# Performance work log

Hardware: AMD Instinct MI355X
Metric: run time of the kernel (lower is better)

The kernel has to match this reference:

```python
import jax, jax.numpy as jnp
import numpy as np

N_NODES = 100000
N_EDGES = 1600000
D_IN = 128
D_HID = 128
D_OUT = 128
N_GRAPHS = 64


def setup_inputs() -> dict:
    key = jax.random.key(0)
    ks = jax.random.split(key, 10)
    x = jax.random.normal(ks[0], (N_NODES, D_IN), dtype=jnp.float32)
    edge_index = jax.random.randint(ks[1], (2, N_EDGES), 0, N_NODES, dtype=jnp.int64)
    graph_id = jnp.sort(jax.random.randint(ks[2], (N_NODES,), 0, N_GRAPHS, dtype=jnp.int64))
    s1 = 1.0 / np.sqrt(D_IN)
    s2 = 1.0 / np.sqrt(D_HID)
    s3 = 1.0 / np.sqrt(D_OUT)
    W1 = jax.random.normal(ks[3], (D_IN, D_HID), dtype=jnp.float32) * s1
    b1 = jnp.zeros((D_HID,), dtype=jnp.float32)
    W2 = jax.random.normal(ks[4], (D_HID, D_OUT), dtype=jnp.float32) * s2
    b2 = jnp.zeros((D_OUT,), dtype=jnp.float32)
    Wr1 = jax.random.normal(ks[5], (D_OUT, D_OUT), dtype=jnp.float32) * s3
    br1 = jnp.zeros((D_OUT,), dtype=jnp.float32)
    Wr2 = jax.random.normal(ks[6], (D_OUT, D_OUT), dtype=jnp.float32) * s3
    br2 = jnp.zeros((D_OUT,), dtype=jnp.float32)
    return {"x": x, "edge_index": edge_index, "graph_id": graph_id,
            "num_graphs": N_GRAPHS, "W1": W1, "b1": b1, "W2": W2, "b2": b2,
            "Wr1": Wr1, "br1": br1, "Wr2": Wr2, "br2": br2}


def _graph_conv(h, W, b, src, dst, norm_src, norm_dst, n_nodes):
    # DGL GraphConv, norm='both': out = D_dst^{-1/2} A (D_src^{-1/2} h) W + b
    h = h * norm_src[:, None]
    h = h @ W  # project first (cheap, keeps SpMM on the smaller/equal dim)
    agg = jax.ops.segment_sum(h[src], dst, num_segments=n_nodes)
    return agg * norm_dst[:, None] + b


def reference(x, edge_index, graph_id, num_graphs, W1, b1, W2, b2, Wr1, br1, Wr2, br2):
    src, dst = edge_index[0], edge_index[1]
    n_nodes = x.shape[0]
    ones = jnp.ones((src.shape[0],), dtype=x.dtype)
    deg_out = jax.ops.segment_sum(ones, src, num_segments=n_nodes)
    deg_in = jax.ops.segment_sum(ones, dst, num_segments=n_nodes)
    norm_src = jnp.clip(deg_out, 1.0) ** -0.5
    norm_dst = jnp.clip(deg_in, 1.0) ** -0.5

    # layer 1 + relu (dropout is identity in eval mode)
    h = _graph_conv(x, W1, b1, src, dst, norm_src, norm_dst, n_nodes)
    h = jax.nn.relu(h)
    # layer 2 + relu
    h = _graph_conv(h, W2, b2, src, dst, norm_src, norm_dst, n_nodes)
    h = jax.nn.relu(h)

    # per-graph mean pooling (dgl.mean_nodes)
    sums = jax.ops.segment_sum(h, graph_id, num_segments=num_graphs)
    counts = jax.ops.segment_sum(jnp.ones((n_nodes,), dtype=h.dtype), graph_id,
                                 num_segments=num_graphs)
    hg = sums / jnp.clip(counts, 1.0)[:, None]

    # readout MLP: Linear -> ReLU -> Linear
    out = jax.nn.relu(hg @ Wr1 + br1) @ Wr2 + br2
    return (out, h)
```

## Files before the change

### kernel.cpp

```cpp
#include <hip/hip_runtime.h>
#include <math.h>


#define D 128
#define BSH 8
#define BKT 256
#define CAP 4608
#define SCHUNK 3200

typedef _Float16 half8 __attribute__((ext_vector_type(8)));
typedef _Float16 half4v __attribute__((ext_vector_type(4)));
typedef _Float16 half2v __attribute__((ext_vector_type(2)));
typedef float f32x4 __attribute__((ext_vector_type(4)));

union H8 { half8 v; half2v h[4]; };

__global__ __launch_bounds__(512) void k_build(const int* __restrict__ src,
                                               const int* __restrict__ dst,
                                               int* __restrict__ cnt_d,
                                               int* __restrict__ cnt_s,
                                               int* __restrict__ packed_d,
                                               unsigned char* __restrict__ packed_s8,
                                               const float* __restrict__ W1,
                                               const float* __restrict__ W2,
                                               _Float16* __restrict__ Wt1,
                                               _Float16* __restrict__ Wt2,
                                               const int* __restrict__ gid,
                                               int* __restrict__ gptr,
                                               int N, int E, int nbkt) {
  __shared__ int hd[512], hs[512], exd[512], exs[512], based[512], bases[512];
  __shared__ int sd[SCHUNK];
  __shared__ unsigned char ss[SCHUNK];
  const int t = threadIdx.x;
  const int bid = blockIdx.x;

  for (int idx = bid * 512 + t; idx < 2 * 128 * 128; idx += gridDim.x * 512) {
    int m = idx >> 14, i = idx & 16383;
    int k = i >> 7, n = i & 127;
    (m ? Wt2 : Wt1)[n * 128 + k] = (_Float16)((m ? W2 : W1)[i]);
  }
  if (bid == gridDim.x - 1 && t <= 64) {
    int lo = 0, hi = N;
    while (lo < hi) {
      int m = (lo + hi) >> 1;
      if (gid[m] < t) lo = m + 1; else hi = m;
    }
    gptr[t] = lo;
  }

  hd[t] = 0; hs[t] = 0;
  __syncthreads();
  const int chunk = (E + gridDim.x - 1) / gridDim.x;
  const int lo = bid * chunk, hi = min(lo + chunk, E);
  const int n = hi - lo;
  for (int i = lo + t; i < hi; i += 512) {
    atomicAdd(&hd[dst[i] >> BSH], 1);
    atomicAdd(&hs[src[i] >> BSH], 1);
  }
  __syncthreads();
  int cD = hd[t], cS = hs[t];
  for (int off = 1; off < 512; off <<= 1) {
    int ad = (t >= off) ? hd[t - off] : 0;
    int as = (t >= off) ? hs[t - off] : 0;
    __syncthreads();
    hd[t] += ad; hs[t] += as;
    __syncthreads();
  }
  exd[t] = hd[t] - cD;
  exs[t] = hs[t] - cS;
  if (t < nbkt) {
    based[t] = cD ? atomicAdd(&cnt_d[t], cD) : 0;
    bases[t] = cS ? atomicAdd(&cnt_s[t], cS) : 0;
  }
  __syncthreads();
  hd[t] = 0; hs[t] = 0;
  __syncthreads();
  for (int i = lo + t; i < hi; i += 512) {
    int s = src[i], d = dst[i];
    int b1 = d >> BSH;
    int r1 = atomicAdd(&hd[b1], 1);
    sd[exd[b1] + r1] = ((d & (BKT - 1)) << 17) | s;
    int b2 = s >> BSH;
    int r2 = atomicAdd(&hs[b2], 1);
    ss[exs[b2] + r2] = (unsigned char)(s & (BKT - 1));
  }
  __syncthreads();
  for (int i = t; i < n; i += 512) {
    int blo = 0, bhi = nbkt - 1;
    while (blo < bhi) {
      int m = (blo + bhi + 1) >> 1;
      if (exd[m] <= i) blo = m; else bhi = m - 1;
    }
    int p = based[blo] + (i - exd[blo]);
    if (p < CAP) packed_d[blo * CAP + p] = sd[i];
    blo = 0; bhi = nbkt - 1;
    while (blo < bhi) {
      int m = (blo + bhi + 1) >> 1;
      if (exs[m] <= i) blo = m; else bhi = m - 1;
    }
    p = bases[blo] + (i - exs[blo]);
    if (p < CAP) packed_s8[blo * CAP + p] = ss[i];
  }
}

union FineLds {
  struct { int excl[256]; int ecache[CAP]; int sorted[CAP]; } d;
  struct { _Float16 As[64][136]; _Float16 Cs[64][128]; } s;
};

__global__ __launch_bounds__(512) void k_fine(const int* __restrict__ packed_d,
                                              const int* __restrict__ cnt_d,
                                              int* __restrict__ row_lo,
                                              int* __restrict__ row_hi,
                                              int* __restrict__ csr,
                                              const unsigned char* __restrict__ packed_s8,
                                              const int* __restrict__ cnt_s,
                                              float* __restrict__ norm_src,
                                              const float* __restrict__ x,
                                              const _Float16* __restrict__ Wt1,
                                              _Float16* __restrict__ P,
                                              int N, int nbkt) {
  __shared__ int hist[256];
  __shared__ FineLds u;
  int t = threadIdx.x;
  if (blockIdx.x >= nbkt) {
    int b = blockIdx.x - nbkt;
    size_t lo = (size_t)b * CAP;
    int cnt = min(cnt_s[b], CAP);
    if (t < 256) hist[t] = 0;
    __syncthreads();
    for (int e = t; e < cnt; e += 512)
      atomicAdd(&hist[packed_s8[lo + e]], 1);
    __syncthreads();
    int nbase = b << BSH;
    if (t < 256 && nbase + t < N)
      norm_src[nbase + t] = rsqrtf(fmaxf((float)hist[t], 1.0f));
    __syncthreads();
    const int l = t & 63;
    const int c = l & 15, quad = l >> 4;
    const int w = t >> 6;
    const int strip = w & 3, chalf = w >> 2;
    for (int ti = 0; ti < 4; ++ti) {
      const int r0 = nbase + ti * 64;
      for (int i = t; i < 64 * 32; i += 512) {
        int r = i >> 5, c4 = i & 31;
        float4 v = {0.f, 0.f, 0.f, 0.f};
        if (r0 + r < N) {
          v = ((const float4*)x)[(size_t)(r0 + r) * 32 + c4];
          float s = rsqrtf(fmaxf((float)hist[ti * 64 + r], 1.0f));
          v.x *= s; v.y *= s; v.z *= s; v.w *= s;
        }
        half4v h = {(_Float16)v.x, (_Float16)v.y, (_Float16)v.z, (_Float16)v.w};
        *(half4v*)&u.s.As[r][c4 * 4] = h;
      }
      __syncthreads();
      f32x4 acc[4];
#pragma unroll
      for (int nt = 0; nt < 4; ++nt) acc[nt] = (f32x4){0.f, 0.f, 0.f, 0.f};
#pragma unroll
      for (int kc = 0; kc < 4; ++kc) {
        half8 a = *(const half8*)&u.s.As[strip * 16 + c][kc * 32 + quad * 8];
#pragma unroll
        for (int nt = 0; nt < 4; ++nt) {
          half8 bb = *(const half8*)&Wt1[(size_t)(chalf * 64 + nt * 16 + c) * 128 + kc * 32 + quad * 8];
          acc[nt] = __builtin_amdgcn_mfma_f32_16x16x32_f16(a, bb, acc[nt], 0, 0, 0);
        }
      }
#pragma unroll
      for (int nt = 0; nt < 4; ++nt)
#pragma unroll
        for (int r = 0; r < 4; ++r)
          u.s.Cs[strip * 16 + quad * 4 + r][chalf * 64 + nt * 16 + c] = (_Float16)acc[nt][r];
      __syncthreads();
      for (int i = t; i < 64 * 16; i += 512) {
        int r = i >> 4, c8 = i & 15;
        if (r0 + r < N)
          ((half8*)P)[(size_t)(r0 + r) * 16 + c8] = *(half8*)&u.s.Cs[r][c8 * 8];
      }
      __syncthreads();
    }
    return;
  }
  int b = blockIdx.x;
  int lo = b * CAP;
  int cnt = min(cnt_d[b], CAP);
  if (t < 256) hist[t] = 0;
  __syncthreads();
  for (int e = t; e < cnt; e += 512) {
    int p = packed_d[lo + e];
    u.d.ecache[e] = p;
    atomicAdd(&hist[p >> 17], 1);
  }
  __syncthreads();
  int v = (t < 256) ? hist[t] : 0;
  for (int off = 1; off < 256; off <<= 1) {
    int a = (t >= off && t < 256) ? hist[t - off] : 0;
    __syncthreads();
    if (t < 256) hist[t] += a;
    __syncthreads();
  }
  int nbase = b << BSH;
  if (t < 256) {
    u.d.excl[t] = hist[t] - v;
    if (nbase + t < N) {
      row_lo[nbase + t] = lo + hist[t] - v;
      row_hi[nbase + t] = lo + hist[t];
    }
  }
  __syncthreads();
  if (t < 256) hist[t] = 0;
  __syncthreads();
  for (int e = t; e < cnt; e += 512) {
    int p = u.d.ecache[e];
    int dlow = p >> 17;
    int r = atomicAdd(&hist[dlow], 1);
    u.d.sorted[u.d.excl[dlow] + r] = p & 0x1FFFF;
  }
  __syncthreads();
  for (int e = t; e < cnt; e += 512)
    csr[lo + e] = u.d.sorted[e];
}

#define PK_ROW(u)                                                           \
  _Pragma("unroll")                                                         \
  for (int k = 0; k < 4; ++k) acch[k] += (u).h[k];

__device__ __forceinline__ void gather_core(const half8* __restrict__ P8,
                                            const int* __restrict__ csr,
                                            int start, int end, int cg, int eg,
                                            int lane, float* acc) {
  half2v acch[4] = {{(_Float16)0.f, (_Float16)0.f}, {(_Float16)0.f, (_Float16)0.f},
                    {(_Float16)0.f, (_Float16)0.f}, {(_Float16)0.f, (_Float16)0.f}};
  for (int s0 = start; s0 < end; s0 += 64) {
    int cnt = min(64, end - s0);
    int idx = (s0 + lane < end) ? csr[s0 + lane] : 0;
    int base = 0;
    for (; base + 16 <= cnt; base += 16) {
      int i0 = __shfl(idx, base + eg);
      int i1 = __shfl(idx, base + 4 + eg);
      int i2 = __shfl(idx, base + 8 + eg);
      int i3 = __shfl(idx, base + 12 + eg);
      H8 u0, u1, u2, u3;
      u0.v = P8[(size_t)i0 * 16 + cg];
      u1.v = P8[(size_t)i1 * 16 + cg];
      u2.v = P8[(size_t)i2 * 16 + cg];
      u3.v = P8[(size_t)i3 * 16 + cg];
      PK_ROW(u0) PK_ROW(u1) PK_ROW(u2) PK_ROW(u3)
    }
    for (; base + 4 <= cnt; base += 4) {
      int i0 = __shfl(idx, base + eg);
      H8 u0;
      u0.v = P8[(size_t)i0 * 16 + cg];
      PK_ROW(u0)
    }
    if (base < cnt) {
      int j = min(base + eg, cnt - 1);
      int i0 = __shfl(idx, j);
      if (base + eg < cnt) {
        H8 u0;
        u0.v = P8[(size_t)i0 * 16 + cg];
        PK_ROW(u0)
      }
    }
  }
#pragma unroll
  for (int k = 0; k < 4; ++k) {
    acc[2 * k]     = (float)acch[k].x;
    acc[2 * k + 1] = (float)acch[k].y;
  }
#pragma unroll
  for (int j = 0; j < 8; ++j) {
    acc[j] += __shfl_xor(acc[j], 16);
    acc[j] += __shfl_xor(acc[j], 32);
  }
}

__global__ __launch_bounds__(256) void k_g1g2(const half8* __restrict__ P8,
                                              const int* __restrict__ row_lo,
                                              const int* __restrict__ row_hi,
                                              const int* __restrict__ csr,
                                              const float* __restrict__ bias,
                                              const float* __restrict__ norm_src,
                                              const _Float16* __restrict__ Wt2,
                                              _Float16* __restrict__ P2, int N) {
  __shared__ _Float16 As[16][136];
  __shared__ _Float16 Cs[16][128];
  const int t = threadIdx.x;
  const int w = t >> 6, lane = t & 63;
  const int cg = lane & 15, eg = lane >> 4;
  const int r0 = blockIdx.x * 16;
  float2 b = ((const float2*)bias)[cg * 4 + eg];
  for (int j = 0; j < 4; ++j) {
    int row = w * 4 + j;
    int wid = r0 + row;
    half2v o = {(_Float16)0.f, (_Float16)0.f};
    if (wid < N) {
      int start = row_lo[wid], end = row_hi[wid];
      float acc[8];
      gather_core(P8, csr, start, end, cg, eg, lane, acc);
      float nd = rsqrtf(fmaxf((float)(end - start), 1.0f));
      float ns = norm_src[wid];
      o.x = (_Float16)(fmaxf(acc[eg * 2] * nd + b.x, 0.f) * ns);
      o.y = (_Float16)(fmaxf(acc[eg * 2 + 1] * nd + b.y, 0.f) * ns);
    }
    *(half2v*)&As[row][2 * (cg * 4 + eg)] = o;
  }
  __syncthreads();
  const int c = cg, quad = eg;
  f32x4 acc[2];
#pragma unroll
  for (int nt = 0; nt < 2; ++nt) acc[nt] = (f32x4){0.f, 0.f, 0.f, 0.f};
#pragma unroll
  for (int kc = 0; kc < 4; ++kc) {
    half8 a = *(const half8*)&As[c][kc * 32 + quad * 8];
#pragma unroll
    for (int nt = 0; nt < 2; ++nt) {
      half8 bb = *(const half8*)&Wt2[(size_t)(w * 32 + nt * 16 + c) * 128 + kc * 32 + quad * 8];
      acc[nt] = __builtin_amdgcn_mfma_f32_16x16x32_f16(a, bb, acc[nt], 0, 0, 0);
    }
  }
#pragma unroll
  for (int nt = 0; nt < 2; ++nt)
#pragma unroll
    for (int r = 0; r < 4; ++r)
      Cs[quad * 4 + r][w * 32 + nt * 16 + c] = (_Float16)acc[nt][r];
  __syncthreads();
  {
    int r = t >> 4, c8 = t & 15;
    if (r0 + r < N)
      ((half8*)P2)[(size_t)(r0 + r) * 16 + c8] = *(half8*)&Cs[r][c8 * 8];
  }
}

__global__ __launch_bounds__(256) void k_gather2(const half8* __restrict__ P8,
                                                 const int* __restrict__ row_lo,
                                                 const int* __restrict__ row_hi,
                                                 const int* __restrict__ csr,
                                                 const float* __restrict__ bias,
                                                 float2* __restrict__ outH, int N) {
  int wid = (blockIdx.x * 256 + threadIdx.x) >> 6;
  if (wid >= N) return;
  int lane = threadIdx.x & 63;
  int cg = lane & 15, eg = lane >> 4;
  int start = row_lo[wid], end = row_hi[wid];
  float acc[8];
  gather_core(P8, csr, start, end, cg, eg, lane, acc);
  float nd = rsqrtf(fmaxf((float)(end - start), 1.0f));
  float2 b = ((const float2*)bias)[cg * 4 + eg];
  float2 o;
  o.x = fmaxf(acc[eg * 2] * nd + b.x, 0.f);
  o.y = fmaxf(acc[eg * 2 + 1] * nd + b.y, 0.f);
  outH[(size_t)wid * 64 + cg * 4 + eg] = o;
}

__global__ __launch_bounds__(256) void k_pool(const float* __restrict__ H,
                                              const int* __restrict__ gptr,
                                              float* __restrict__ pool) {
  int g = blockIdx.x >> 3, chunk = blockIdx.x & 7;
  int col = threadIdx.x & 127, rpar = threadIdx.x >> 7;
  int s = gptr[g], e = gptr[g + 1];
  float acc = 0.0f;
  for (int r = s + chunk * 2 + rpar; r < e; r += 16)
    acc += H[(size_t)r * D + col];
  __shared__ float red[256];
  red[threadIdx.x] = acc;
  __syncthreads();
  if (rpar == 0) atomicAdd(&pool[g * D + col], acc + red[threadIdx.x + 128]);
}

__global__ __launch_bounds__(128) void k_readout(const float* __restrict__ pool,
                                                 const int* __restrict__ gptr,
                                                 const float* __restrict__ Wr1,
                                                 const float* __restrict__ br1,
                                                 const float* __restrict__ Wr2,
                                                 const float* __restrict__ br2,
                                                 float* __restrict__ out) {
  int g = blockIdx.x;
  int j = threadIdx.x;
  __shared__ float hg[D];
  __shared__ float t1[D];
  float cnt = fmaxf((float)(gptr[g + 1] - gptr[g]), 1.0f);
  hg[j] = pool[(size_t)g * D + j] / cnt;
  __syncthreads();
  float a = br1[j];
  for (int k = 0; k < D; ++k) a += hg[k] * Wr1[(size_t)k * D + j];
  t1[j] = fmaxf(a, 0.0f);
  __syncthreads();
  float b = br2[j];
  for (int k = 0; k < D; ++k) b += t1[k] * Wr2[(size_t)k * D + j];
  out[(size_t)g * D + j] = b;
}

extern "C" void kernel_launch(void* const* d_in, const int* in_sizes, int n_in,
                              void* d_out, int out_size, void* d_ws, size_t ws_size,
                              hipStream_t stream) {
  const float* x   = (const float*)d_in[0];
  const int* edge  = (const int*)d_in[1];
  const int* gid   = (const int*)d_in[2];
  const float* W1  = (const float*)d_in[4];
  const float* b1  = (const float*)d_in[5];
  const float* W2  = (const float*)d_in[6];
  const float* b2  = (const float*)d_in[7];
  const float* Wr1 = (const float*)d_in[8];
  const float* br1 = (const float*)d_in[9];
  const float* Wr2 = (const float*)d_in[10];
  const float* br2 = (const float*)d_in[11];

  const int N = in_sizes[0] / D;
  const int E = in_sizes[1] / 2;
  const int* src = edge;
  const int* dst = edge + E;
  const int nbkt = (N + BKT - 1) >> BSH;

  float* bufA     = (float*)d_ws;
  float* bufB     = bufA + (size_t)N * D;
  int* row_lo     = (int*)(bufB + (size_t)N * D);
  int* row_hi     = row_lo + N;
  int* csr        = row_hi + N;
  float* norm_src = (float*)(csr + (size_t)nbkt * CAP);
  float* pool     = norm_src + N;
  int* gptr       = (int*)(pool + 64 * D);
  int* cnt_d      = gptr + 65;
  int* cnt_s      = cnt_d + 512;
  _Float16* Wt1   = (_Float16*)(cnt_s + 512);
  _Float16* Wt2   = Wt1 + 128 * 128;
  int* packed_d   = (int*)(bufA + (size_t)N * D / 2);
  unsigned char* packed_s8 = (unsigned char*)(packed_d + (size_t)nbkt * CAP);
  size_t need = ((size_t)2 * N * D + 3 * (size_t)N + (size_t)nbkt * CAP
                 + 64 * D + 65 + 1024 + 16384 + 1024) * sizeof(float);
  if (ws_size < need) return;

  float* out_g = (float*)d_out;
  float* h_out = out_g + 64 * D;

  _Float16* P  = (_Float16*)bufA;
  _Float16* P2 = (_Float16*)bufB;

  hipMemsetAsync(pool, 0, (64 * D + 65 + 1024) * sizeof(float), stream);

  const int build_grid = (E + SCHUNK - 1) / SCHUNK;
  k_build<<<build_grid, 512, 0, stream>>>(src, dst, cnt_d, cnt_s,
                                          packed_d, packed_s8,
                                          W1, W2, Wt1, Wt2, gid, gptr,
                                          N, E, nbkt);
  k_fine<<<2 * nbkt, 512, 0, stream>>>(packed_d, cnt_d, row_lo, row_hi, csr,
                                       packed_s8, cnt_s, norm_src,
                                       x, Wt1, P, N, nbkt);

  k_g1g2<<<(N + 15) / 16, 256, 0, stream>>>(
      (const half8*)P, row_lo, row_hi, csr, b1, norm_src, Wt2, P2, N);

  k_gather2<<<(N * 64 + 255) / 256, 256, 0, stream>>>(
      (const half8*)P2, row_lo, row_hi, csr, b2, (float2*)h_out, N);

  k_pool<<<64 * 8, 256, 0, stream>>>(h_out, gptr, pool);
  k_readout<<<64, 128, 0, stream>>>(pool, gptr, Wr1, br1, Wr2, br2, out_g);
}
```

Measured before the change: 358.3 us.

## Fuse layer-2 gather with mean-pool accumulation and zero pool inside build kernel

Merges the final gather kernel and the separate pooling kernel. Each 1024-thread block handles 16 rows, reduces them in shared memory, and does one atomic per column when all 16 rows share a graph id. Otherwise it falls back to per-element atomics. This removes a kernel launch and the re-read of the full fp32 hidden output for pooling. Zeroing of the pool buffer moves into the build kernel, and the memset shrinks to cover only the counters. The trade-offs are more atomics on the pool buffer and 1024-thread blocks that may lower occupancy for the gather.

```diff
diff --git a/kernel.cpp b/kernel.cpp
--- a/kernel.cpp
+++ b/kernel.cpp
@@ -27,6 +27,7 @@
                                                _Float16* __restrict__ Wt2,
                                                const int* __restrict__ gid,
                                                int* __restrict__ gptr,
+                                               float* __restrict__ pool,
                                                int N, int E, int nbkt) {
   __shared__ int hd[512], hs[512], exd[512], exs[512], based[512], bases[512];
   __shared__ int sd[SCHUNK];
@@ -39,6 +40,8 @@
     int k = i >> 7, n = i & 127;
     (m ? Wt2 : Wt1)[n * 128 + k] = (_Float16)((m ? W2 : W1)[i]);
   }
+  for (int i = bid * 512 + t; i < 64 * D; i += gridDim.x * 512)
+    pool[i] = 0.0f;
   if (bid == gridDim.x - 1 && t <= 64) {
     int lo = 0, hi = N;
     while (lo < hi) {
@@ -332,40 +335,49 @@
   }
 }
 
-__global__ __launch_bounds__(256) void k_gather2(const half8* __restrict__ P8,
+__global__ __launch_bounds__(1024) void k_g2pool(const half8* __restrict__ P8,
                                                  const int* __restrict__ row_lo,
                                                  const int* __restrict__ row_hi,
                                                  const int* __restrict__ csr,
                                                  const float* __restrict__ bias,
-                                                 float2* __restrict__ outH, int N) {
-  int wid = (blockIdx.x * 256 + threadIdx.x) >> 6;
-  if (wid >= N) return;
-  int lane = threadIdx.x & 63;
-  int cg = lane & 15, eg = lane >> 4;
-  int start = row_lo[wid], end = row_hi[wid];
-  float acc[8];
-  gather_core(P8, csr, start, end, cg, eg, lane, acc);
-  float nd = rsqrtf(fmaxf((float)(end - start), 1.0f));
-  float2 b = ((const float2*)bias)[cg * 4 + eg];
-  float2 o;
-  o.x = fmaxf(acc[eg * 2] * nd + b.x, 0.f);
-  o.y = fmaxf(acc[eg * 2 + 1] * nd + b.y, 0.f);
-  outH[(size_t)wid * 64 + cg * 4 + eg] = o;
-}
-
-__global__ __launch_bounds__(256) void k_pool(const float* __restrict__ H,
-                                              const int* __restrict__ gptr,
-                                              float* __restrict__ pool) {
-  int g = blockIdx.x >> 3, chunk = blockIdx.x & 7;
-  int col = threadIdx.x & 127, rpar = threadIdx.x >> 7;
-  int s = gptr[g], e = gptr[g + 1];
-  float acc = 0.0f;
-  for (int r = s + chunk * 2 + rpar; r < e; r += 16)
-    acc += H[(size_t)r * D + col];
-  __shared__ float red[256];
-  red[threadIdx.x] = acc;
-  __syncthreads();
-  if (rpar == 0) atomicAdd(&pool[g * D + col], acc + red[threadIdx.x + 128]);
+                                                 const int* __restrict__ gid,
+                                                 float2* __restrict__ outH,
+                                                 float* __restrict__ pool, int N) {
+  __shared__ float red[16][128];
+  const int t = threadIdx.x;
+  const int w = t >> 6, lane = t & 63;
+  const int cg = lane & 15, eg = lane >> 4;
+  const int r0 = blockIdx.x * 16;
+  const int wid = r0 + w;
+  const int col0 = (cg * 4 + eg) * 2;
+  float2 o = {0.f, 0.f};
+  if (wid < N) {
+    int start = row_lo[wid], end = row_hi[wid];
+    float acc[8];
+    gather_core(P8, csr, start, end, cg, eg, lane, acc);
+    float nd = rsqrtf(fmaxf((float)(end - start), 1.0f));
+    float2 b = ((const float2*)bias)[cg * 4 + eg];
+    o.x = fmaxf(acc[eg * 2] * nd + b.x, 0.f);
+    o.y = fmaxf(acc[eg * 2 + 1] * nd + b.y, 0.f);
+    outH[(size_t)wid * 64 + cg * 4 + eg] = o;
+  }
+  red[w][col0] = o.x;
+  red[w][col0 + 1] = o.y;
+  __syncthreads();
+  int g0 = gid[r0];
+  int g1 = gid[min(r0 + 15, N - 1)];
+  if (g0 == g1) {
+    if (t < 128) {
+      float s = 0.f;
+#pragma unroll
+      for (int k = 0; k < 16; ++k) s += red[k][t];
+      atomicAdd(&pool[g0 * D + t], s);
+    }
+  } else if (wid < N) {
+    int g = gid[wid];
+    atomicAdd(&pool[g * D + col0], o.x);
+    atomicAdd(&pool[g * D + col0 + 1], o.y);
+  }
 }
 
 __global__ __launch_bounds__(128) void k_readout(const float* __restrict__ pool,
@@ -436,12 +448,12 @@
   _Float16* P  = (_Float16*)bufA;
   _Float16* P2 = (_Float16*)bufB;
 
-  hipMemsetAsync(pool, 0, (64 * D + 65 + 1024) * sizeof(float), stream);
+  hipMemsetAsync(cnt_d, 0, 1024 * sizeof(int), stream);
 
   const int build_grid = (E + SCHUNK - 1) / SCHUNK;
   k_build<<<build_grid, 512, 0, stream>>>(src, dst, cnt_d, cnt_s,
                                           packed_d, packed_s8,
-                                          W1, W2, Wt1, Wt2, gid, gptr,
+                                          W1, W2, Wt1, Wt2, gid, gptr, pool,
                                           N, E, nbkt);
   k_fine<<<2 * nbkt, 512, 0, stream>>>(packed_d, cnt_d, row_lo, row_hi, csr,
                                        packed_s8, cnt_s, norm_src,
@@ -450,9 +462,8 @@
   k_g1g2<<<(N + 15) / 16, 256, 0, stream>>>(
       (const half8*)P, row_lo, row_hi, csr, b1, norm_src, Wt2, P2, N);
 
-  k_gather2<<<(N * 64 + 255) / 256, 256, 0, stream>>>(
-      (const half8*)P2, row_lo, row_hi, csr, b2, (float2*)h_out, N);
-
-  k_pool<<<64 * 8, 256, 0, stream>>>(h_out, gptr, pool);
+  k_g2pool<<<(N + 15) / 16, 1024, 0, stream>>>(
+      (const half8*)P2, row_lo, row_hi, csr, b2, gid, (float2*)h_out, pool, N);
+
   k_readout<<<64, 128, 0, stream>>>(pool, gptr, Wr1, br1, Wr2, br2, out_g);
 }
```

Result: faster. 346.3 us (-3.3%).
